# Kernel optimization log

Hardware: AMD Instinct MI355X
Metric: run time of the kernel (lower is better)

## Reference

```python
import jax, jax.numpy as jnp
import numpy as np

N_NODES = 50000
N_EDGES = 1_600_000
IN_DIM = 128
OUT_DIM = 128


def setup_inputs() -> dict:
    key = jax.random.key(0)
    k1, k2, k3, k4, k5, k6 = jax.random.split(key, 6)
    H = jax.random.normal(k1, (N_NODES, IN_DIM), dtype=jnp.float32)
    edge_src = jax.random.randint(k2, (N_EDGES,), 0, N_NODES, dtype=jnp.int32)
    edge_dst = jnp.sort(jax.random.randint(k3, (N_EDGES,), 0, N_NODES, dtype=jnp.int32))
    edge_weight = jax.random.uniform(k4, (N_EDGES,), dtype=jnp.float32)
    bound = np.sqrt(6.0 / (IN_DIM + OUT_DIM))
    W = jax.random.uniform(k5, (IN_DIM, OUT_DIM), dtype=jnp.float32, minval=-bound, maxval=bound)
    b = jax.random.normal(k6, (OUT_DIM,), dtype=jnp.float32)
    return {"H": H, "edge_src": edge_src, "edge_dst": edge_dst,
            "edge_weight": edge_weight, "W": W, "b": b}


def reference(H, edge_src, edge_dst, edge_weight, W, b):
    # A_hat @ H: gather source features, scale by edge weight, scatter-sum to dst.
    msgs = edge_weight[:, None] * jnp.take(H, edge_src, axis=0)   # [E, in_dim]
    agg = jax.ops.segment_sum(msgs, edge_dst, num_segments=N_NODES)  # [N, in_dim]
    # Dense transform + bias (no activation in original forward).
    return agg @ W + b
```

## Files before the change

### kernel.cpp

```cpp
#include <hip/hip_runtime.h>

#define IN_DIM 128
#define OUT_DIM 128

typedef __attribute__((ext_vector_type(8))) short short8v;
typedef __attribute__((ext_vector_type(4))) float float4v;
typedef __attribute__((ext_vector_type(4))) unsigned int uint4v;

__device__ __forceinline__ ushort f2bf(float f) {
    unsigned int u = __builtin_bit_cast(unsigned int, f);
    unsigned int r = (u + 0x7fffu + ((u >> 16) & 1u)) >> 16;
    return (ushort)r;
}

__device__ __forceinline__ unsigned int pk2bf(float x, float y) {
#if __has_builtin(__builtin_amdgcn_cvt_pk_bf16_f32)
    typedef __attribute__((ext_vector_type(2))) __bf16 bf2;
    bf2 r = __builtin_amdgcn_cvt_pk_bf16_f32(x, y);
    return __builtin_bit_cast(unsigned int, r);
#else
    return (unsigned int)f2bf(x) | ((unsigned int)f2bf(y) << 16);
#endif
}

__global__ __launch_bounds__(256) void prep_kernel(const float* __restrict__ W,
                                                   ushort* __restrict__ Wt) {
    int k0 = blockIdx.x * 8;
    int n = threadIdx.x & 127;
    int half = threadIdx.x >> 7;
#pragma unroll
    for (int kp = 0; kp < 2; ++kp) {
        int k = k0 + (half * 2 + kp) * 2;
        float v0 = W[k * 128 + n];
        float v1 = W[(k + 1) * 128 + n];
        *(unsigned int*)&Wt[n * 136 + k] = pk2bf(v0, v1);
    }
}

__global__ __launch_bounds__(256) void gemm_kernel(const float* __restrict__ H,
                                                   const ushort* __restrict__ Wt_g,
                                                   unsigned char* __restrict__ T8,
                                                   float* __restrict__ S, int M,
                                                   const int* __restrict__ edst,
                                                   int* __restrict__ rp,
                                                   int E, int nb_gemm) {
    __shared__ ushort Ws[128 * 136];

    const int t = threadIdx.x;

    if (blockIdx.x >= nb_gemm) {
        int n = (blockIdx.x - nb_gemm) * 256 + t;
        if (n <= M) {
            int lo = 0, hi = E;
            while (lo < hi) {
                int mid = (lo + hi) >> 1;
                if (edst[mid] < n) lo = mid + 1; else hi = mid;
            }
            rp[n] = lo;
        }
        return;
    }

    const int row0 = blockIdx.x * 64;

#pragma unroll
    for (int f = t; f < 2176; f += 256)
        ((short8v*)Ws)[f] = ((const short8v*)Wt_g)[f];

    const int w = t >> 6;
    const int l = t & 63;
    const int m16 = l & 15;
    const int kq = (l >> 4) * 8;
    const int gr = row0 + w * 16 + m16;

    float4 h[8];
    if (gr < M) {
#pragma unroll
        for (int ks = 0; ks < 4; ++ks) {
            h[ks * 2]     = *(const float4*)&H[gr * 128 + ks * 32 + kq];
            h[ks * 2 + 1] = *(const float4*)&H[gr * 128 + ks * 32 + kq + 4];
        }
    } else {
#pragma unroll
        for (int i = 0; i < 8; ++i) h[i] = make_float4(0.f, 0.f, 0.f, 0.f);
    }

    short8v bfrag[4];
#pragma unroll
    for (int ks = 0; ks < 4; ++ks) {
        uint4v u;
        u[0] = pk2bf(h[ks * 2].x, h[ks * 2].y);
        u[1] = pk2bf(h[ks * 2].z, h[ks * 2].w);
        u[2] = pk2bf(h[ks * 2 + 1].x, h[ks * 2 + 1].y);
        u[3] = pk2bf(h[ks * 2 + 1].z, h[ks * 2 + 1].w);
        bfrag[ks] = __builtin_bit_cast(short8v, u);
    }

    __syncthreads();

    float4v acc[8];
#pragma unroll
    for (int nt = 0; nt < 8; ++nt) acc[nt] = (float4v){0.f, 0.f, 0.f, 0.f};

#pragma unroll
    for (int ks = 0; ks < 4; ++ks) {
#pragma unroll
        for (int nt = 0; nt < 8; ++nt) {
            short8v afrag = *(const short8v*)&Ws[(nt * 16 + m16) * 136 + ks * 32 + kq];
            acc[nt] = __builtin_amdgcn_mfma_f32_16x16x32_bf16(afrag, bfrag[ks], acc[nt], 0, 0, 0);
        }
    }

    float mx = 0.f;
#pragma unroll
    for (int nt = 0; nt < 8; ++nt) {
#pragma unroll
        for (int k = 0; k < 4; ++k) mx = fmaxf(mx, fabsf(acc[nt][k]));
    }
    mx = fmaxf(mx, __shfl_xor(mx, 16));
    mx = fmaxf(mx, __shfl_xor(mx, 32));

    const float inv = 127.0f / fmaxf(mx, 1e-20f);

    if (gr < M) {
        const int qd = l >> 4;
        if (qd == 0) S[gr] = mx * (1.0f / 127.0f);
#pragma unroll
        for (int nt = 0; nt < 8; ++nt) {
            unsigned int p = 0;
#pragma unroll
            for (int k = 0; k < 4; ++k) {
                int qi = (int)__builtin_rintf(acc[nt][k] * inv);
                qi = qi > 127 ? 127 : (qi < -127 ? -127 : qi);
                p |= ((unsigned int)(qi + 128) & 0xffu) << (k * 8);
            }
            *(unsigned int*)&T8[gr * 128 + nt * 16 + qd * 4] = p;
        }
    }
}

__global__ __launch_bounds__(256) void scatter_kernel(const ushort* __restrict__ T16,
                                                      const float* __restrict__ S,
                                                      const int* __restrict__ esrc,
                                                      const float* __restrict__ ew,
                                                      const int* __restrict__ rp,
                                                      const float* __restrict__ b,
                                                      float* __restrict__ out) {
    const int node = blockIdx.x * 4 + (threadIdx.x >> 6);
    const int lane = threadIdx.x & 63;

    const int s = __builtin_amdgcn_readfirstlane(rp[node]);
    const int e = __builtin_amdgcn_readfirstlane(rp[node + 1]);

    float ax = 0.f, ay = 0.f;
    float B = 0.f;

    for (int c = s; c < e; c += 64) {
        const int idx = c + lane;
        int srcl = 0;
        float wl = 0.f;
        if (idx < e) { srcl = esrc[idx]; wl = ew[idx]; }
        const float wsl = wl * S[srcl];
        const int wsbits = __builtin_bit_cast(int, wsl);
        int nn = e - c;
        if (nn > 64) nn = 64;

        for (int j = 0; j < nn; j += 8) {
            int sq[8];
            float wq[8];
            ushort vv[8];
#pragma unroll
            for (int q = 0; q < 8; ++q) {
                sq[q] = __builtin_amdgcn_readlane(srcl, j + q);
                wq[q] = __builtin_bit_cast(float,
                            __builtin_amdgcn_readlane(wsbits, j + q));
            }
#pragma unroll
            for (int q = 0; q < 8; ++q)
                vv[q] = T16[(unsigned int)sq[q] * 64u + (unsigned int)lane];
#pragma unroll
            for (int q = 0; q < 8; ++q) {
                unsigned int v = vv[q];
                B += wq[q];
                ax = fmaf((float)(v & 0xffu), wq[q], ax);
                ay = fmaf((float)((v >> 8) & 0xffu), wq[q], ay);
            }
        }
    }

    float2 bias = *(const float2*)&b[lane * 2];
    float ox = fmaf(-128.0f, B, ax) + bias.x;
    float oy = fmaf(-128.0f, B, ay) + bias.y;

    *(float2*)&out[node * 128 + lane * 2] = make_float2(ox, oy);
}

extern "C" void kernel_launch(void* const* d_in, const int* in_sizes, int n_in,
                              void* d_out, int out_size, void* d_ws, size_t ws_size,
                              hipStream_t stream) {
    const float* H    = (const float*)d_in[0];
    const int*   esrc = (const int*)d_in[1];
    const int*   edst = (const int*)d_in[2];
    const float* ew   = (const float*)d_in[3];
    const float* W    = (const float*)d_in[4];
    const float* b    = (const float*)d_in[5];
    float* out = (float*)d_out;

    const int M = in_sizes[0] / IN_DIM;
    const int E = in_sizes[1];

    unsigned char* T8 = (unsigned char*)d_ws;
    size_t off = (size_t)M * 128;
    float* S  = (float*)((char*)d_ws + off);
    off += (size_t)M * 4;
    ushort* Wt = (ushort*)((char*)d_ws + off);
    off += 128 * 136 * 2;
    int* rp = (int*)((char*)d_ws + off);

    prep_kernel<<<16, 256, 0, stream>>>(W, Wt);

    const int nb_gemm = (M + 63) / 64;
    const int nb_rp   = (M + 1 + 255) / 256;
    gemm_kernel<<<nb_gemm + nb_rp, 256, 0, stream>>>(H, Wt, T8, S, M, edst, rp, E, nb_gemm);

    scatter_kernel<<<(M + 3) / 4, 256, 0, stream>>>((const ushort*)T8, S, esrc, ew, rp, b, out);
}
```

Baseline: 139.3 us.

## Split wave into two half-waves loading 4-byte rows for two edges at once

The scatter kernel now has each half of a wavefront handle a different edge. Each lane loads 4 bytes (4 int8 features) instead of 2, so one gather instruction covers two source rows. Partial sums from the two halves are combined with a cross-half shuffle before a float4 store. This cuts the number of gather loads per edge in half, at the cost of shuffles instead of scalar readlanes, per-lane divergent source addresses, and half the lanes sitting idle at the store.

```diff
diff --git a/kernel.cpp b/kernel.cpp
--- a/kernel.cpp
+++ b/kernel.cpp
@@ -139,7 +139,7 @@
     }
 }
 
-__global__ __launch_bounds__(256) void scatter_kernel(const ushort* __restrict__ T16,
+__global__ __launch_bounds__(256) void scatter_kernel(const unsigned char* __restrict__ T8,
                                                       const float* __restrict__ S,
                                                       const int* __restrict__ esrc,
                                                       const float* __restrict__ ew,
@@ -148,11 +148,13 @@
                                                       float* __restrict__ out) {
     const int node = blockIdx.x * 4 + (threadIdx.x >> 6);
     const int lane = threadIdx.x & 63;
+    const int half = lane >> 5;
+    const unsigned int colb = (lane & 31u) * 4u;
 
     const int s = __builtin_amdgcn_readfirstlane(rp[node]);
     const int e = __builtin_amdgcn_readfirstlane(rp[node + 1]);
 
-    float ax = 0.f, ay = 0.f;
+    float ax0 = 0.f, ax1 = 0.f, ax2 = 0.f, ax3 = 0.f;
     float B = 0.f;
 
     for (int c = s; c < e; c += 64) {
@@ -161,38 +163,50 @@
         float wl = 0.f;
         if (idx < e) { srcl = esrc[idx]; wl = ew[idx]; }
         const float wsl = wl * S[srcl];
-        const int wsbits = __builtin_bit_cast(int, wsl);
         int nn = e - c;
         if (nn > 64) nn = 64;
 
         for (int j = 0; j < nn; j += 8) {
-            int sq[8];
-            float wq[8];
-            ushort vv[8];
-#pragma unroll
-            for (int q = 0; q < 8; ++q) {
-                sq[q] = __builtin_amdgcn_readlane(srcl, j + q);
-                wq[q] = __builtin_bit_cast(float,
-                            __builtin_amdgcn_readlane(wsbits, j + q));
-            }
-#pragma unroll
-            for (int q = 0; q < 8; ++q)
-                vv[q] = T16[(unsigned int)sq[q] * 64u + (unsigned int)lane];
-#pragma unroll
-            for (int q = 0; q < 8; ++q) {
-                unsigned int v = vv[q];
-                B += wq[q];
-                ax = fmaf((float)(v & 0xffu), wq[q], ax);
-                ay = fmaf((float)((v >> 8) & 0xffu), wq[q], ay);
-            }
-        }
-    }
-
-    float2 bias = *(const float2*)&b[lane * 2];
-    float ox = fmaf(-128.0f, B, ax) + bias.x;
-    float oy = fmaf(-128.0f, B, ay) + bias.y;
-
-    *(float2*)&out[node * 128 + lane * 2] = make_float2(ox, oy);
+            int sqp[4];
+            float wsp[4];
+            unsigned int vv[4];
+#pragma unroll
+            for (int p = 0; p < 4; ++p) {
+                const int srcLane = j + p * 2 + half;
+                sqp[p] = __shfl(srcl, srcLane);
+                wsp[p] = __shfl(wsl, srcLane);
+            }
+#pragma unroll
+            for (int p = 0; p < 4; ++p)
+                vv[p] = *(const unsigned int*)(T8 + ((unsigned int)sqp[p] * 128u + colb));
+#pragma unroll
+            for (int p = 0; p < 4; ++p) {
+                const unsigned int v = vv[p];
+                const float ws = wsp[p];
+                B += ws;
+                ax0 = fmaf((float)(v & 0xffu), ws, ax0);
+                ax1 = fmaf((float)((v >> 8) & 0xffu), ws, ax1);
+                ax2 = fmaf((float)((v >> 16) & 0xffu), ws, ax2);
+                ax3 = fmaf((float)(v >> 24), ws, ax3);
+            }
+        }
+    }
+
+    ax0 += __shfl_xor(ax0, 32);
+    ax1 += __shfl_xor(ax1, 32);
+    ax2 += __shfl_xor(ax2, 32);
+    ax3 += __shfl_xor(ax3, 32);
+    B   += __shfl_xor(B, 32);
+
+    if (half == 0) {
+        const float4 bb = *(const float4*)&b[colb];
+        float4 o;
+        o.x = fmaf(-128.0f, B, ax0) + bb.x;
+        o.y = fmaf(-128.0f, B, ax1) + bb.y;
+        o.z = fmaf(-128.0f, B, ax2) + bb.z;
+        o.w = fmaf(-128.0f, B, ax3) + bb.w;
+        *(float4*)&out[node * 128 + colb] = o;
+    }
 }
 
 extern "C" void kernel_launch(void* const* d_in, const int* in_sizes, int n_in,
@@ -223,5 +237,5 @@
     const int nb_rp   = (M + 1 + 255) / 256;
     gemm_kernel<<<nb_gemm + nb_rp, 256, 0, stream>>>(H, Wt, T8, S, M, edst, rp, E, nb_gemm);
 
-    scatter_kernel<<<(M + 3) / 4, 256, 0, stream>>>((const ushort*)T8, S, esrc, ew, rp, b, out);
-}
+    scatter_kernel<<<(M + 3) / 4, 256, 0, stream>>>(T8, S, esrc, ew, rp, b, out);
+}
```

New measurement: 132.9 us, median of 2. 1.05x faster.

## Split wave into quarters that each gather 8-byte slices of four edge rows

Applied to the files above, without the earlier changes.

The scatter kernel now splits each 64-lane wave into four 16-lane quarters. Each quarter loads an 8-byte slice of a different source row, so a single wave-wide load covers four edges instead of one. Up to four batches of gathers are issued before any decoding, which puts more memory requests in flight per wave. Partial sums are combined across quarters with shuffles and only one quarter writes the output. The cost is more accumulator registers, per-lane shuffles in place of scalar readlanes, and a cross-lane reduction at the end.

```diff
diff --git a/kernel.cpp b/kernel.cpp
--- a/kernel.cpp
+++ b/kernel.cpp
@@ -6,6 +6,7 @@
 typedef __attribute__((ext_vector_type(8))) short short8v;
 typedef __attribute__((ext_vector_type(4))) float float4v;
 typedef __attribute__((ext_vector_type(4))) unsigned int uint4v;
+typedef __attribute__((ext_vector_type(2))) unsigned int uint2v;
 
 __device__ __forceinline__ ushort f2bf(float f) {
     unsigned int u = __builtin_bit_cast(unsigned int, f);
@@ -139,7 +140,39 @@
     }
 }
 
-__global__ __launch_bounds__(256) void scatter_kernel(const ushort* __restrict__ T16,
+#define ISSUE_BATCH(J, SQ, WS, V)                                              \
+    {                                                                          \
+        _Pragma("unroll")                                                      \
+        for (int p = 0; p < 4; ++p) {                                          \
+            const int sl = (J) + p * 4 + quarter;                              \
+            SQ[p] = __shfl(srcl, sl);                                          \
+            WS[p] = __shfl(wsl, sl);                                           \
+        }                                                                      \
+        _Pragma("unroll")                                                      \
+        for (int p = 0; p < 4; ++p)                                            \
+            V[p] = *(const uint2v*)(T8 + ((unsigned int)SQ[p] * 128u + colb)); \
+    }
+
+#define DECODE_BATCH(WS, V)                                                    \
+    {                                                                          \
+        _Pragma("unroll")                                                      \
+        for (int p = 0; p < 4; ++p) {                                          \
+            const unsigned int x = V[p][0];                                    \
+            const unsigned int y = V[p][1];                                    \
+            const float w = WS[p];                                             \
+            B  += w;                                                           \
+            a0 = fmaf((float)(x & 0xffu), w, a0);                              \
+            a1 = fmaf((float)((x >> 8) & 0xffu), w, a1);                       \
+            a2 = fmaf((float)((x >> 16) & 0xffu), w, a2);                      \
+            a3 = fmaf((float)(x >> 24), w, a3);                                \
+            a4 = fmaf((float)(y & 0xffu), w, a4);                              \
+            a5 = fmaf((float)((y >> 8) & 0xffu), w, a5);                       \
+            a6 = fmaf((float)((y >> 16) & 0xffu), w, a6);                      \
+            a7 = fmaf((float)(y >> 24), w, a7);                                \
+        }                                                                      \
+    }
+
+__global__ __launch_bounds__(256) void scatter_kernel(const unsigned char* __restrict__ T8,
                                                       const float* __restrict__ S,
                                                       const int* __restrict__ esrc,
                                                       const float* __restrict__ ew,
@@ -148,11 +181,14 @@
                                                       float* __restrict__ out) {
     const int node = blockIdx.x * 4 + (threadIdx.x >> 6);
     const int lane = threadIdx.x & 63;
+    const int quarter = lane >> 4;
+    const unsigned int colb = (lane & 15u) * 8u;
 
     const int s = __builtin_amdgcn_readfirstlane(rp[node]);
     const int e = __builtin_amdgcn_readfirstlane(rp[node + 1]);
 
-    float ax = 0.f, ay = 0.f;
+    float a0 = 0.f, a1 = 0.f, a2 = 0.f, a3 = 0.f;
+    float a4 = 0.f, a5 = 0.f, a6 = 0.f, a7 = 0.f;
     float B = 0.f;
 
     for (int c = s; c < e; c += 64) {
@@ -161,38 +197,51 @@
         float wl = 0.f;
         if (idx < e) { srcl = esrc[idx]; wl = ew[idx]; }
         const float wsl = wl * S[srcl];
-        const int wsbits = __builtin_bit_cast(int, wsl);
         int nn = e - c;
         if (nn > 64) nn = 64;
-
-        for (int j = 0; j < nn; j += 8) {
-            int sq[8];
-            float wq[8];
-            ushort vv[8];
-#pragma unroll
-            for (int q = 0; q < 8; ++q) {
-                sq[q] = __builtin_amdgcn_readlane(srcl, j + q);
-                wq[q] = __builtin_bit_cast(float,
-                            __builtin_amdgcn_readlane(wsbits, j + q));
-            }
-#pragma unroll
-            for (int q = 0; q < 8; ++q)
-                vv[q] = T16[(unsigned int)sq[q] * 64u + (unsigned int)lane];
-#pragma unroll
-            for (int q = 0; q < 8; ++q) {
-                unsigned int v = vv[q];
-                B += wq[q];
-                ax = fmaf((float)(v & 0xffu), wq[q], ax);
-                ay = fmaf((float)((v >> 8) & 0xffu), wq[q], ay);
-            }
-        }
-    }
-
-    float2 bias = *(const float2*)&b[lane * 2];
-    float ox = fmaf(-128.0f, B, ax) + bias.x;
-    float oy = fmaf(-128.0f, B, ay) + bias.y;
-
-    *(float2*)&out[node * 128 + lane * 2] = make_float2(ox, oy);
+        const int nb = (nn + 15) >> 4;
+
+        int   sq0[4], sq1[4], sq2[4], sq3[4];
+        float ws0[4], ws1[4], ws2[4], ws3[4];
+        uint2v v0[4], v1[4], v2[4], v3[4];
+
+        ISSUE_BATCH(0, sq0, ws0, v0);
+        if (nb > 1) ISSUE_BATCH(16, sq1, ws1, v1);
+        if (nb > 2) ISSUE_BATCH(32, sq2, ws2, v2);
+        if (nb > 3) ISSUE_BATCH(48, sq3, ws3, v3);
+
+        DECODE_BATCH(ws0, v0);
+        if (nb > 1) DECODE_BATCH(ws1, v1);
+        if (nb > 2) DECODE_BATCH(ws2, v2);
+        if (nb > 3) DECODE_BATCH(ws3, v3);
+    }
+
+    a0 += __shfl_xor(a0, 16); a0 += __shfl_xor(a0, 32);
+    a1 += __shfl_xor(a1, 16); a1 += __shfl_xor(a1, 32);
+    a2 += __shfl_xor(a2, 16); a2 += __shfl_xor(a2, 32);
+    a3 += __shfl_xor(a3, 16); a3 += __shfl_xor(a3, 32);
+    a4 += __shfl_xor(a4, 16); a4 += __shfl_xor(a4, 32);
+    a5 += __shfl_xor(a5, 16); a5 += __shfl_xor(a5, 32);
+    a6 += __shfl_xor(a6, 16); a6 += __shfl_xor(a6, 32);
+    a7 += __shfl_xor(a7, 16); a7 += __shfl_xor(a7, 32);
+    B  += __shfl_xor(B, 16);  B  += __shfl_xor(B, 32);
+
+    if (quarter == 0) {
+        const int col = (lane & 15) * 8;
+        const float4 b0 = *(const float4*)&b[col];
+        const float4 b1 = *(const float4*)&b[col + 4];
+        float4 o0, o1;
+        o0.x = fmaf(-128.0f, B, a0) + b0.x;
+        o0.y = fmaf(-128.0f, B, a1) + b0.y;
+        o0.z = fmaf(-128.0f, B, a2) + b0.z;
+        o0.w = fmaf(-128.0f, B, a3) + b0.w;
+        o1.x = fmaf(-128.0f, B, a4) + b1.x;
+        o1.y = fmaf(-128.0f, B, a5) + b1.y;
+        o1.z = fmaf(-128.0f, B, a6) + b1.z;
+        o1.w = fmaf(-128.0f, B, a7) + b1.w;
+        *(float4*)&out[node * 128 + col]     = o0;
+        *(float4*)&out[node * 128 + col + 4] = o1;
+    }
 }
 
 extern "C" void kernel_launch(void* const* d_in, const int* in_sizes, int n_in,
@@ -223,5 +272,5 @@
     const int nb_rp   = (M + 1 + 255) / 256;
     gemm_kernel<<<nb_gemm + nb_rp, 256, 0, stream>>>(H, Wt, T8, S, M, edst, rp, E, nb_gemm);
 
-    scatter_kernel<<<(M + 3) / 4, 256, 0, stream>>>((const ushort*)T8, S, esrc, ew, rp, b, out);
-}
+    scatter_kernel<<<(M + 3) / 4, 256, 0, stream>>>(T8, S, esrc, ew, rp, b, out);
+}
```

After: 136.8 us. Within noise of the previous version (-1.8%).
